# Performance work log

Measured on AMD Instinct MI355X. Metric: run time of the kernel, lower is better.

Reference implementation:

```python
import jax, jax.numpy as jnp
import numpy as np

N = 100000
E = 1600000
IN, HID, OUT = 64, 128, 64
EPS = 1e-5


def _sage_conv(x, src, dst, w_l, b_l, w_r):
    # PyG SAGEConv (mean aggr): out = lin_l(mean_{j in N(i)} x_j) + lin_r(x_i)
    msgs = x[src]                                   # [E, d] gather
    agg = jax.ops.segment_sum(msgs, dst, num_segments=N)  # [N, d]
    deg = jax.ops.segment_sum(jnp.ones((E,), x.dtype), dst, num_segments=N)
    agg = agg / jnp.maximum(deg, 1.0)[:, None]      # mean over neighbors
    return agg @ w_l.T + b_l + x @ w_r.T


def _bn_eval(x, gamma, beta, mean, var):
    return (x - mean) * jax.lax.rsqrt(var + EPS) * gamma + beta


def setup_inputs() -> dict:
    key = jax.random.key(0)
    ks = jax.random.split(key, 16)
    x = jax.random.normal(ks[0], (N, IN), jnp.float32)
    edge_index = jax.random.randint(ks[1], (2, E), 0, N, jnp.int32)
    s1 = 1.0 / np.sqrt(IN)
    s2 = 1.0 / np.sqrt(HID)
    return {
        "x": x,
        "edge_index": edge_index,
        "w1l": jax.random.uniform(ks[2], (HID, IN), jnp.float32, -s1, s1),
        "b1l": jax.random.uniform(ks[3], (HID,), jnp.float32, -s1, s1),
        "w1r": jax.random.uniform(ks[4], (HID, IN), jnp.float32, -s1, s1),
        "bn1_gamma": jax.random.uniform(ks[5], (HID,), jnp.float32, 0.5, 1.5),
        "bn1_beta": jax.random.normal(ks[6], (HID,), jnp.float32) * 0.1,
        "bn1_mean": jax.random.normal(ks[7], (HID,), jnp.float32) * 0.1,
        "bn1_var": jax.random.uniform(ks[8], (HID,), jnp.float32, 0.5, 1.5),
        "w2l": jax.random.uniform(ks[9], (OUT, HID), jnp.float32, -s2, s2),
        "b2l": jax.random.uniform(ks[10], (OUT,), jnp.float32, -s2, s2),
        "w2r": jax.random.uniform(ks[11], (OUT, HID), jnp.float32, -s2, s2),
        "bn2_gamma": jax.random.uniform(ks[12], (OUT,), jnp.float32, 0.5, 1.5),
        "bn2_beta": jax.random.normal(ks[13], (OUT,), jnp.float32) * 0.1,
        "bn2_mean": jax.random.normal(ks[14], (OUT,), jnp.float32) * 0.1,
        "bn2_var": jax.random.uniform(ks[15], (OUT,), jnp.float32, 0.5, 1.5),
    }


def reference(x, edge_index, w1l, b1l, w1r, bn1_gamma, bn1_beta, bn1_mean, bn1_var,
              w2l, b2l, w2r, bn2_gamma, bn2_beta, bn2_mean, bn2_var):
    src, dst = edge_index[0], edge_index[1]
    # layer 1: SAGEConv -> BN -> ReLU (dropout is identity in eval mode)
    h = _sage_conv(x, src, dst, w1l, b1l, w1r)
    h = jax.nn.relu(_bn_eval(h, bn1_gamma, bn1_beta, bn1_mean, bn1_var))
    # layer 2: SAGEConv -> BN
    h = _sage_conv(h, src, dst, w2l, b2l, w2r)
    return _bn_eval(h, bn2_gamma, bn2_beta, bn2_mean, bn2_var)
```

## Files before the change

### kernel.cpp

```cpp
#include <hip/hip_runtime.h>

#define NN 100000
#define NE 1600000
#define EPSV 1e-5f

#define NBUK 196
#define TILE 2048
#define NTIL 782
#define CAP  9216

typedef __attribute__((ext_vector_type(8))) short bf16x8;
typedef __attribute__((ext_vector_type(4))) float f32x4;

__device__ inline unsigned short f2bf(float f) {
  unsigned u = __builtin_bit_cast(unsigned, f);
  unsigned r = u + 0x7FFFu + ((u >> 16) & 1u);
  return (unsigned short)(r >> 16);
}
__device__ inline float bf2f(unsigned short s) {
  unsigned u = ((unsigned)s) << 16;
  return __builtin_bit_cast(float, u);
}

__global__ __launch_bounds__(256) void k_bin(const int* __restrict__ src,
                                             const int* __restrict__ dst,
                                             unsigned* __restrict__ pairs,
                                             int* __restrict__ tileCnt,
                                             int* __restrict__ tileLo) {
  __shared__ int cnt[NBUK];
  __shared__ int lo[NBUK];
  __shared__ int ts[256];
  __shared__ unsigned stage[TILE];
  const int tid = threadIdx.x;
  const int t = blockIdx.x;
  const int e0 = t * TILE;
  const int m = min(TILE, NE - e0);

  for (int i = tid; i < NBUK; i += 256) cnt[i] = 0;
  __syncthreads();
  for (int i = tid; i < m; i += 256) {
    atomicAdd(&cnt[dst[e0 + i] >> 9], 1);
  }
  __syncthreads();
  int c = (tid < NBUK) ? cnt[tid] : 0;
  ts[tid] = c;
  __syncthreads();
  for (int d = 1; d < 256; d <<= 1) {
    int v = (tid >= d) ? ts[tid - d] : 0;
    __syncthreads();
    ts[tid] += v;
    __syncthreads();
  }
  if (tid < NBUK) {
    int ex = ts[tid] - c;
    lo[tid] = ex;
    cnt[tid] = ex;
  }
  __syncthreads();
  for (int i = tid; i < m; i += 256) {
    int d = dst[e0 + i];
    int s = src[e0 + i];
    int pos = atomicAdd(&cnt[d >> 9], 1);
    stage[pos] = ((unsigned)(d & 511) << 17) | (unsigned)s;
  }
  __syncthreads();
  for (int i = tid; i < m; i += 256) pairs[(size_t)t * TILE + i] = stage[i];
  if (tid < NBUK) {
    tileCnt[t * NBUK + tid] = cnt[tid] - lo[tid];
    tileLo[t * NBUK + tid] = lo[tid];
  }
}

__global__ __launch_bounds__(256) void k_colscan(const int* __restrict__ tileCnt,
                                                 int* __restrict__ colBase,
                                                 int* __restrict__ total) {
  __shared__ int ts[256];
  const int tid = threadIdx.x;
  const int b = blockIdx.x;
  int v[4];
  int s = 0;
#pragma unroll
  for (int j = 0; j < 4; ++j) {
    int tt = tid * 4 + j;
    v[j] = (tt < NTIL) ? tileCnt[tt * NBUK + b] : 0;
    s += v[j];
  }
  ts[tid] = s;
  __syncthreads();
  for (int d = 1; d < 256; d <<= 1) {
    int x = (tid >= d) ? ts[tid - d] : 0;
    __syncthreads();
    ts[tid] += x;
    __syncthreads();
  }
  int run = ts[tid] - s;
#pragma unroll
  for (int j = 0; j < 4; ++j) {
    int tt = tid * 4 + j;
    if (tt < NTIL) colBase[(size_t)b * NTIL + tt] = run;
    run += v[j];
  }
  if (tid == 255) total[b] = ts[255];
}

__global__ __launch_bounds__(256) void k_bscan(const int* __restrict__ total,
                                               int* __restrict__ bucketBase) {
  __shared__ int ts[256];
  const int tid = threadIdx.x;
  int c = (tid < NBUK) ? min(total[tid], CAP) : 0;
  ts[tid] = c;
  __syncthreads();
  for (int d = 1; d < 256; d <<= 1) {
    int v = (tid >= d) ? ts[tid - d] : 0;
    __syncthreads();
    ts[tid] += v;
    __syncthreads();
  }
  if (tid < NBUK) bucketBase[tid] = ts[tid] - c;
}

__global__ __launch_bounds__(512) void k_build(const unsigned* __restrict__ pairs,
                                               const int* __restrict__ tileLo,
                                               const int* __restrict__ colBase,
                                               const int* __restrict__ total,
                                               const int* __restrict__ bucketBase,
                                               int* __restrict__ deg,
                                               int* __restrict__ offset,
                                               int* __restrict__ csr) {
  __shared__ unsigned stageA[CAP];
  __shared__ unsigned stageB[CAP];
  __shared__ int colB[NTIL];
  __shared__ int tLo[NTIL];
  __shared__ int hist[512];
  __shared__ int ts[512];
  const int tid = threadIdx.x;
  const int b = blockIdx.x;
  const int count = min(total[b], CAP);
  const int nbase = b * 512;
  const int nloc = min(512, NN - nbase);
  const int obase = bucketBase[b];

  for (int i = tid; i < NTIL; i += 512) {
    colB[i] = colBase[(size_t)b * NTIL + i];
    tLo[i] = tileLo[i * NBUK + b];
  }
  hist[tid] = 0;
  __syncthreads();
  for (int i = tid; i < count; i += 512) {
    int a = 0, z = NTIL - 1;
    while (a < z) {
      int mid = (a + z + 1) >> 1;
      if (colB[mid] <= i) a = mid; else z = mid - 1;
    }
    stageA[i] = pairs[(size_t)a * TILE + tLo[a] + (i - colB[a])];
  }
  __syncthreads();
  for (int i = tid; i < count; i += 512) {
    atomicAdd(&hist[stageA[i] >> 17], 1);
  }
  __syncthreads();
  int s = hist[tid];
  ts[tid] = s;
  __syncthreads();
  for (int d = 1; d < 512; d <<= 1) {
    int v = (tid >= d) ? ts[tid - d] : 0;
    __syncthreads();
    ts[tid] += v;
    __syncthreads();
  }
  int ex = ts[tid] - s;
  if (tid < nloc) {
    deg[nbase + tid] = s;
    offset[nbase + tid] = obase + ex;
  }
  hist[tid] = ex;
  __syncthreads();
  for (int i = tid; i < count; i += 512) {
    unsigned e = stageA[i];
    int pos = atomicAdd(&hist[e >> 17], 1);
    stageB[pos] = e & 0x1FFFFu;
  }
  __syncthreads();
  for (int i = tid; i < count; i += 512) csr[obase + i] = (int)stageB[i];
}

__global__ __launch_bounds__(256) void k_prep(const float* __restrict__ x,
                                              unsigned short* __restrict__ xb,
                                              const float* __restrict__ w1l,
                                              const float* __restrict__ w1r,
                                              const float* __restrict__ w2l,
                                              const float* __restrict__ w2r,
                                              const float* __restrict__ b1l,
                                              const float* __restrict__ g1,
                                              const float* __restrict__ be1,
                                              const float* __restrict__ m1,
                                              const float* __restrict__ v1,
                                              const float* __restrict__ b2l,
                                              const float* __restrict__ g2,
                                              const float* __restrict__ be2,
                                              const float* __restrict__ m2,
                                              const float* __restrict__ v2,
                                              unsigned short* __restrict__ w1c,
                                              unsigned short* __restrict__ w2c,
                                              float* __restrict__ bn) {
  int gi = blockIdx.x * 256 + threadIdx.x;
  float4 v = *(const float4*)(x + (size_t)gi * 4);
  ushort4 o;
  o.x = f2bf(v.x); o.y = f2bf(v.y); o.z = f2bf(v.z); o.w = f2bf(v.w);
  *(ushort4*)(xb + (size_t)gi * 4) = o;
  if (blockIdx.x < 64) {
    int i = gi;
    int oo = i >> 7, k = i & 127;
    float vv1 = (k < 64) ? w1l[oo * 64 + k] : w1r[oo * 64 + (k - 64)];
    w1c[i] = f2bf(vv1);
    float vv2 = (oo < 64) ? w2l[oo * 128 + k] : w2r[(oo - 64) * 128 + k];
    w2c[i] = f2bf(vv2);
    if (i < 128) {
      float sc = g1[i] * rsqrtf(v1[i] + EPSV);
      bn[i] = sc;
      bn[128 + i] = (b1l[i] - m1[i]) * sc + be1[i];
    }
    if (i < 64) {
      float sc = g2[i] * rsqrtf(v2[i] + EPSV);
      bn[256 + i] = sc;
      bn[320 + i] = (b2l[i] - m2[i]) * sc + be2[i];
    }
  }
}

__global__ __launch_bounds__(256) void k_aggregate(const unsigned short* __restrict__ xb,
                                                   const int* __restrict__ deg,
                                                   const int* __restrict__ offset,
                                                   const int* __restrict__ csr,
                                                   unsigned short* __restrict__ aggB) {
  int tid = threadIdx.x;
  int node = blockIdx.x * 32 + (tid >> 3);
  int j = tid & 7;
  int cnt = deg[node];
  const int* arow = csr + offset[node];
  float a0=0.f,a1=0.f,a2=0.f,a3=0.f,a4=0.f,a5=0.f,a6=0.f,a7=0.f;
  int k = 0;
  for (; k + 4 <= cnt; k += 4) {
    int s0 = arow[k], s1 = arow[k+1], s2 = arow[k+2], s3 = arow[k+3];
    uint4 v0 = *(const uint4*)(xb + (size_t)s0 * 64 + j * 8);
    uint4 v1 = *(const uint4*)(xb + (size_t)s1 * 64 + j * 8);
    uint4 v2 = *(const uint4*)(xb + (size_t)s2 * 64 + j * 8);
    uint4 v3 = *(const uint4*)(xb + (size_t)s3 * 64 + j * 8);
    a0 += bf2f(v0.x & 0xffff) + bf2f(v1.x & 0xffff) + bf2f(v2.x & 0xffff) + bf2f(v3.x & 0xffff);
    a1 += bf2f(v0.x >> 16)    + bf2f(v1.x >> 16)    + bf2f(v2.x >> 16)    + bf2f(v3.x >> 16);
    a2 += bf2f(v0.y & 0xffff) + bf2f(v1.y & 0xffff) + bf2f(v2.y & 0xffff) + bf2f(v3.y & 0xffff);
    a3 += bf2f(v0.y >> 16)    + bf2f(v1.y >> 16)    + bf2f(v2.y >> 16)    + bf2f(v3.y >> 16);
    a4 += bf2f(v0.z & 0xffff) + bf2f(v1.z & 0xffff) + bf2f(v2.z & 0xffff) + bf2f(v3.z & 0xffff);
    a5 += bf2f(v0.z >> 16)    + bf2f(v1.z >> 16)    + bf2f(v2.z >> 16)    + bf2f(v3.z >> 16);
    a6 += bf2f(v0.w & 0xffff) + bf2f(v1.w & 0xffff) + bf2f(v2.w & 0xffff) + bf2f(v3.w & 0xffff);
    a7 += bf2f(v0.w >> 16)    + bf2f(v1.w >> 16)    + bf2f(v2.w >> 16)    + bf2f(v3.w >> 16);
  }
  for (; k < cnt; ++k) {
    int s = arow[k];
    uint4 v = *(const uint4*)(xb + (size_t)s * 64 + j * 8);
    a0 += bf2f(v.x & 0xffff); a1 += bf2f(v.x >> 16);
    a2 += bf2f(v.y & 0xffff); a3 += bf2f(v.y >> 16);
    a4 += bf2f(v.z & 0xffff); a5 += bf2f(v.z >> 16);
    a6 += bf2f(v.w & 0xffff); a7 += bf2f(v.w >> 16);
  }
  float inv = 1.0f / fmaxf((float)cnt, 1.0f);
  ushort4 r0, r1;
  r0.x = f2bf(a0 * inv); r0.y = f2bf(a1 * inv); r0.z = f2bf(a2 * inv); r0.w = f2bf(a3 * inv);
  r1.x = f2bf(a4 * inv); r1.y = f2bf(a5 * inv); r1.z = f2bf(a6 * inv); r1.w = f2bf(a7 * inv);
  *(ushort4*)(aggB + (size_t)node * 64 + j * 8) = r0;
  *(ushort4*)(aggB + (size_t)node * 64 + j * 8 + 4) = r1;
}

__global__ __launch_bounds__(256) void k_gemm12(const unsigned short* __restrict__ aggB,
                                                const unsigned short* __restrict__ xb,
                                                const unsigned short* __restrict__ w1c,
                                                const unsigned short* __restrict__ w2c,
                                                const float* __restrict__ bn,
                                                unsigned short* __restrict__ t,
                                                unsigned short* __restrict__ r2) {
  __shared__ unsigned short wlds[32 * 512];
  __shared__ unsigned short hlds[4][2][16 * 128];
  __shared__ float bnlds[384];
  const int tid = threadIdx.x;
  const int w = tid >> 6;
  const int lane = tid & 63;
  const int lr = lane & 15;
  const int q = lane >> 4;
  const int base = blockIdx.x * 128 + w * 32;
  const int nA = base + lr, nB = base + 16 + lr;
  const int cA = min(nA, NN - 1), cB = min(nB, NN - 1);
  const int swz = (lr & 7) << 4;

  bf16x8 fA[4], fB[4];
  {
    const unsigned short* a = aggB + (size_t)cA * 64 + q * 8;
    const unsigned short* xx = xb + (size_t)cA * 64 + q * 8;
    fA[0] = *(const bf16x8*)a;        fA[1] = *(const bf16x8*)(a + 32);
    fA[2] = *(const bf16x8*)xx;       fA[3] = *(const bf16x8*)(xx + 32);
  }
  {
    const unsigned short* a = aggB + (size_t)cB * 64 + q * 8;
    const unsigned short* xx = xb + (size_t)cB * 64 + q * 8;
    fB[0] = *(const bf16x8*)a;        fB[1] = *(const bf16x8*)(a + 32);
    fB[2] = *(const bf16x8*)xx;       fB[3] = *(const bf16x8*)(xx + 32);
  }

  for (int i = tid; i < 384; i += 256) bnlds[i] = bn[i];
  for (int idx = tid; idx < 2048; idx += 256) {
    int f = idx >> 6, l = idx & 63;
    int gofs = ((f >> 2) * 16 + (l & 15)) * 128 + (f & 3) * 32 + (l >> 4) * 8;
    *(uint4*)&wlds[idx * 8] = *(const uint4*)&w1c[gofs];
  }
  __syncthreads();

  char* ldsA = (char*)&hlds[w][0][0];
  char* ldsB = (char*)&hlds[w][1][0];

#pragma unroll
  for (int ot = 0; ot < 8; ++ot) {
    const unsigned short* wp = &wlds[(ot * 4) * 512 + lane * 8];
    bf16x8 w0 = *(const bf16x8*)(wp);
    bf16x8 w1 = *(const bf16x8*)(wp + 512);
    bf16x8 w2 = *(const bf16x8*)(wp + 1024);
    bf16x8 w3 = *(const bf16x8*)(wp + 1536);
    f32x4 aA = {0.f, 0.f, 0.f, 0.f}, aB = {0.f, 0.f, 0.f, 0.f};
    aA = __builtin_amdgcn_mfma_f32_16x16x32_bf16(w0, fA[0], aA, 0, 0, 0);
    aA = __builtin_amdgcn_mfma_f32_16x16x32_bf16(w1, fA[1], aA, 0, 0, 0);
    aA = __builtin_amdgcn_mfma_f32_16x16x32_bf16(w2, fA[2], aA, 0, 0, 0);
    aA = __builtin_amdgcn_mfma_f32_16x16x32_bf16(w3, fA[3], aA, 0, 0, 0);
    aB = __builtin_amdgcn_mfma_f32_16x16x32_bf16(w0, fB[0], aB, 0, 0, 0);
    aB = __builtin_amdgcn_mfma_f32_16x16x32_bf16(w1, fB[1], aB, 0, 0, 0);
    aB = __builtin_amdgcn_mfma_f32_16x16x32_bf16(w2, fB[2], aB, 0, 0, 0);
    aB = __builtin_amdgcn_mfma_f32_16x16x32_bf16(w3, fB[3], aB, 0, 0, 0);
    const int o = ot * 16 + q * 4;
    float4 sc = *(const float4*)&bnlds[o];
    float4 sh = *(const float4*)&bnlds[128 + o];
    ushort4 hA, hB;
    hA.x = f2bf(fmaxf(aA[0] * sc.x + sh.x, 0.f));
    hA.y = f2bf(fmaxf(aA[1] * sc.y + sh.y, 0.f));
    hA.z = f2bf(fmaxf(aA[2] * sc.z + sh.z, 0.f));
    hA.w = f2bf(fmaxf(aA[3] * sc.w + sh.w, 0.f));
    hB.x = f2bf(fmaxf(aB[0] * sc.x + sh.x, 0.f));
    hB.y = f2bf(fmaxf(aB[1] * sc.y + sh.y, 0.f));
    hB.z = f2bf(fmaxf(aB[2] * sc.z + sh.z, 0.f));
    hB.w = f2bf(fmaxf(aB[3] * sc.w + sh.w, 0.f));
    const int wb = lr * 256 + ot * 32 + q * 8;
    *(ushort4*)(ldsA + (wb ^ swz)) = hA;
    *(ushort4*)(ldsB + (wb ^ swz)) = hB;
  }
  __syncthreads();

  for (int idx = tid; idx < 2048; idx += 256) {
    int f = idx >> 6, l = idx & 63;
    int gofs = ((f >> 2) * 16 + (l & 15)) * 128 + (f & 3) * 32 + (l >> 4) * 8;
    *(uint4*)&wlds[idx * 8] = *(const uint4*)&w2c[gofs];
  }
  __syncthreads();

  bf16x8 hA[4], hB[4];
#pragma unroll
  for (int jj = 0; jj < 4; ++jj) {
    const int rb = lr * 256 + jj * 64 + q * 16;
    hA[jj] = *(const bf16x8*)(ldsA + (rb ^ swz));
    hB[jj] = *(const bf16x8*)(ldsB + (rb ^ swz));
  }

#pragma unroll
  for (int ot = 0; ot < 8; ++ot) {
    const unsigned short* wp = &wlds[(ot * 4) * 512 + lane * 8];
    bf16x8 w0 = *(const bf16x8*)(wp);
    bf16x8 w1 = *(const bf16x8*)(wp + 512);
    bf16x8 w2 = *(const bf16x8*)(wp + 1024);
    bf16x8 w3 = *(const bf16x8*)(wp + 1536);
    f32x4 aA = {0.f, 0.f, 0.f, 0.f}, aB = {0.f, 0.f, 0.f, 0.f};
    aA = __builtin_amdgcn_mfma_f32_16x16x32_bf16(w0, hA[0], aA, 0, 0, 0);
    aA = __builtin_amdgcn_mfma_f32_16x16x32_bf16(w1, hA[1], aA, 0, 0, 0);
    aA = __builtin_amdgcn_mfma_f32_16x16x32_bf16(w2, hA[2], aA, 0, 0, 0);
    aA = __builtin_amdgcn_mfma_f32_16x16x32_bf16(w3, hA[3], aA, 0, 0, 0);
    aB = __builtin_amdgcn_mfma_f32_16x16x32_bf16(w0, hB[0], aB, 0, 0, 0);
    aB = __builtin_amdgcn_mfma_f32_16x16x32_bf16(w1, hB[1], aB, 0, 0, 0);
    aB = __builtin_amdgcn_mfma_f32_16x16x32_bf16(w2, hB[2], aB, 0, 0, 0);
    aB = __builtin_amdgcn_mfma_f32_16x16x32_bf16(w3, hB[3], aB, 0, 0, 0);
    ushort4 tv;
    if (ot < 4) {
      const int o = ot * 16 + q * 4;
      tv.x = f2bf(aA[0]); tv.y = f2bf(aA[1]); tv.z = f2bf(aA[2]); tv.w = f2bf(aA[3]);
      if (nA < NN) *(ushort4*)(t + (size_t)nA * 64 + o) = tv;
      tv.x = f2bf(aB[0]); tv.y = f2bf(aB[1]); tv.z = f2bf(aB[2]); tv.w = f2bf(aB[3]);
      if (nB < NN) *(ushort4*)(t + (size_t)nB * 64 + o) = tv;
    } else {
      const int o = (ot - 4) * 16 + q * 4;
      tv.x = f2bf(aA[0]); tv.y = f2bf(aA[1]); tv.z = f2bf(aA[2]); tv.w = f2bf(aA[3]);
      if (nA < NN) *(ushort4*)(r2 + (size_t)nA * 64 + o) = tv;
      tv.x = f2bf(aB[0]); tv.y = f2bf(aB[1]); tv.z = f2bf(aB[2]); tv.w = f2bf(aB[3]);
      if (nB < NN) *(ushort4*)(r2 + (size_t)nB * 64 + o) = tv;
    }
  }
}

__global__ __launch_bounds__(256) void k_agg2fin(const unsigned short* __restrict__ t,
                                                 const int* __restrict__ deg,
                                                 const int* __restrict__ offset,
                                                 const int* __restrict__ csr,
                                                 const unsigned short* __restrict__ r2,
                                                 const float* __restrict__ bn,
                                                 float* __restrict__ outp) {
  int tid = threadIdx.x;
  int node = blockIdx.x * 32 + (tid >> 3);
  int j = tid & 7;
  int cnt = deg[node];
  const int* arow = csr + offset[node];
  float a0=0.f,a1=0.f,a2=0.f,a3=0.f,a4=0.f,a5=0.f,a6=0.f,a7=0.f;
  int k = 0;
  for (; k + 4 <= cnt; k += 4) {
    int s0 = arow[k], s1 = arow[k+1], s2 = arow[k+2], s3 = arow[k+3];
    uint4 v0 = *(const uint4*)(t + (size_t)s0 * 64 + j * 8);
    uint4 v1 = *(const uint4*)(t + (size_t)s1 * 64 + j * 8);
    uint4 v2 = *(const uint4*)(t + (size_t)s2 * 64 + j * 8);
    uint4 v3 = *(const uint4*)(t + (size_t)s3 * 64 + j * 8);
    a0 += bf2f(v0.x & 0xffff) + bf2f(v1.x & 0xffff) + bf2f(v2.x & 0xffff) + bf2f(v3.x & 0xffff);
    a1 += bf2f(v0.x >> 16)    + bf2f(v1.x >> 16)    + bf2f(v2.x >> 16)    + bf2f(v3.x >> 16);
    a2 += bf2f(v0.y & 0xffff) + bf2f(v1.y & 0xffff) + bf2f(v2.y & 0xffff) + bf2f(v3.y & 0xffff);
    a3 += bf2f(v0.y >> 16)    + bf2f(v1.y >> 16)    + bf2f(v2.y >> 16)    + bf2f(v3.y >> 16);
    a4 += bf2f(v0.z & 0xffff) + bf2f(v1.z & 0xffff) + bf2f(v2.z & 0xffff) + bf2f(v3.z & 0xffff);
    a5 += bf2f(v0.z >> 16)    + bf2f(v1.z >> 16)    + bf2f(v2.z >> 16)    + bf2f(v3.z >> 16);
    a6 += bf2f(v0.w & 0xffff) + bf2f(v1.w & 0xffff) + bf2f(v2.w & 0xffff) + bf2f(v3.w & 0xffff);
    a7 += bf2f(v0.w >> 16)    + bf2f(v1.w >> 16)    + bf2f(v2.w >> 16)    + bf2f(v3.w >> 16);
  }
  for (; k < cnt; ++k) {
    int s = arow[k];
    uint4 v = *(const uint4*)(t + (size_t)s * 64 + j * 8);
    a0 += bf2f(v.x & 0xffff); a1 += bf2f(v.x >> 16);
    a2 += bf2f(v.y & 0xffff); a3 += bf2f(v.y >> 16);
    a4 += bf2f(v.z & 0xffff); a5 += bf2f(v.z >> 16);
    a6 += bf2f(v.w & 0xffff); a7 += bf2f(v.w >> 16);
  }
  float inv = 1.0f / fmaxf((float)cnt, 1.0f);
  int o = j * 8;
  uint4 rv = *(const uint4*)(r2 + (size_t)node * 64 + o);
  float r0 = bf2f(rv.x & 0xffff), r1 = bf2f(rv.x >> 16);
  float r2a = bf2f(rv.y & 0xffff), r3 = bf2f(rv.y >> 16);
  float r4 = bf2f(rv.z & 0xffff), r5 = bf2f(rv.z >> 16);
  float r6 = bf2f(rv.w & 0xffff), r7 = bf2f(rv.w >> 16);
  float4 sca = *(const float4*)(bn + 256 + o);
  float4 scb = *(const float4*)(bn + 256 + o + 4);
  float4 sha = *(const float4*)(bn + 320 + o);
  float4 shb = *(const float4*)(bn + 320 + o + 4);
  float4 o0, o1;
  o0.x = (a0 * inv + r0) * sca.x + sha.x;
  o0.y = (a1 * inv + r1) * sca.y + sha.y;
  o0.z = (a2 * inv + r2a) * sca.z + sha.z;
  o0.w = (a3 * inv + r3) * sca.w + sha.w;
  o1.x = (a4 * inv + r4) * scb.x + shb.x;
  o1.y = (a5 * inv + r5) * scb.y + shb.y;
  o1.z = (a6 * inv + r6) * scb.z + shb.z;
  o1.w = (a7 * inv + r7) * scb.w + shb.w;
  *(float4*)(outp + (size_t)node * 64 + o) = o0;
  *(float4*)(outp + (size_t)node * 64 + o + 4) = o1;
}

extern "C" void kernel_launch(void* const* d_in, const int* in_sizes, int n_in,
                              void* d_out, int out_size, void* d_ws, size_t ws_size,
                              hipStream_t stream) {
  const float* x   = (const float*)d_in[0];
  const int*   ei  = (const int*)d_in[1];
  const float* w1l = (const float*)d_in[2];
  const float* b1l = (const float*)d_in[3];
  const float* w1r = (const float*)d_in[4];
  const float* g1  = (const float*)d_in[5];
  const float* be1 = (const float*)d_in[6];
  const float* m1  = (const float*)d_in[7];
  const float* v1  = (const float*)d_in[8];
  const float* w2l = (const float*)d_in[9];
  const float* b2l = (const float*)d_in[10];
  const float* w2r = (const float*)d_in[11];
  const float* g2  = (const float*)d_in[12];
  const float* be2 = (const float*)d_in[13];
  const float* m2  = (const float*)d_in[14];
  const float* v2  = (const float*)d_in[15];
  float* outp = (float*)d_out;

  char* ws = (char*)d_ws;
  int*            tileCnt    = (int*)ws;
  int*            tileLo     = (int*)(ws + 613120);
  int*            colBase    = (int*)(ws + 1226240);
  int*            total      = (int*)(ws + 1839360);
  int*            bucketBase = (int*)(ws + 1840384);
  int*            deg        = (int*)(ws + 1841408);
  int*            offset     = (int*)(ws + 2241408);
  unsigned*       pairs      = (unsigned*)(ws + 2641408);
  int*            csr        = (int*)(ws + 9047552);
  unsigned short* w1c        = (unsigned short*)(ws + 15447552);
  unsigned short* w2c        = (unsigned short*)(ws + 15480320);
  float*          bn         = (float*)(ws + 15513088);
  unsigned short* xb         = (unsigned short*)(ws + 15515136);
  unsigned short* aggB       = (unsigned short*)(ws + 28315136);
  unsigned short* t          = (unsigned short*)(ws + 41115136);
  unsigned short* r2         = (unsigned short*)(ws + 53915136);

  const int* srcp = ei;
  const int* dstp = ei + NE;

  hipLaunchKernelGGL(k_prep, dim3(NN * 64 / 1024), dim3(256), 0, stream,
                     x, xb, w1l, w1r, w2l, w2r, b1l, g1, be1, m1, v1,
                     b2l, g2, be2, m2, v2, w1c, w2c, bn);
  hipLaunchKernelGGL(k_bin, dim3(NTIL), dim3(256), 0, stream,
                     srcp, dstp, pairs, tileCnt, tileLo);
  hipLaunchKernelGGL(k_colscan, dim3(NBUK), dim3(256), 0, stream,
                     tileCnt, colBase, total);
  hipLaunchKernelGGL(k_bscan, dim3(1), dim3(256), 0, stream, total, bucketBase);
  hipLaunchKernelGGL(k_build, dim3(NBUK), dim3(512), 0, stream,
                     pairs, tileLo, colBase, total, bucketBase, deg, offset, csr);
  hipLaunchKernelGGL(k_aggregate, dim3(NN / 32), dim3(256), 0, stream,
                     xb, deg, offset, csr, aggB);
  hipLaunchKernelGGL(k_gemm12, dim3((NN + 127) / 128), dim3(256), 0, stream,
                     aggB, xb, w1c, w2c, bn, t, r2);
  hipLaunchKernelGGL(k_agg2fin, dim3(NN / 32), dim3(256), 0, stream,
                     t, deg, offset, csr, r2, bn, outp);
}
```

Before: 140.4 us.

## Preload both weight matrices into LDS via direct global-to-LDS loads

k_gemm12 now allocates separate LDS buffers for both weight matrices and loads them up front with global_load_lds, removing the mid-kernel reload of w2 and two block barriers. Blocks grow to 512 threads (8 waves) with launch_bounds(512,1), halving the number of blocks that each load the weights. In exchange, LDS use per block roughly doubles, which may cap occupancy. Per-wave h tiles stay private, so the barrier between layers is no longer needed.

```diff
diff --git a/kernel.cpp b/kernel.cpp
--- a/kernel.cpp
+++ b/kernel.cpp
@@ -20,6 +20,12 @@
 __device__ inline float bf2f(unsigned short s) {
   unsigned u = ((unsigned)s) << 16;
   return __builtin_bit_cast(float, u);
+}
+
+__device__ __forceinline__ void gload_lds16(const unsigned short* g, unsigned short* l) {
+  __builtin_amdgcn_global_load_lds(
+      (const __attribute__((address_space(1))) void*)g,
+      (__attribute__((address_space(3))) void*)l, 16, 0, 0);
 }
 
 __global__ __launch_bounds__(256) void k_bin(const int* __restrict__ src,
@@ -271,25 +277,37 @@
   *(ushort4*)(aggB + (size_t)node * 64 + j * 8 + 4) = r1;
 }
 
-__global__ __launch_bounds__(256) void k_gemm12(const unsigned short* __restrict__ aggB,
-                                                const unsigned short* __restrict__ xb,
-                                                const unsigned short* __restrict__ w1c,
-                                                const unsigned short* __restrict__ w2c,
-                                                const float* __restrict__ bn,
-                                                unsigned short* __restrict__ t,
-                                                unsigned short* __restrict__ r2) {
-  __shared__ unsigned short wlds[32 * 512];
-  __shared__ unsigned short hlds[4][2][16 * 128];
+__global__ __launch_bounds__(512, 1) void k_gemm12(const unsigned short* __restrict__ aggB,
+                                                   const unsigned short* __restrict__ xb,
+                                                   const unsigned short* __restrict__ w1c,
+                                                   const unsigned short* __restrict__ w2c,
+                                                   const float* __restrict__ bn,
+                                                   unsigned short* __restrict__ t,
+                                                   unsigned short* __restrict__ r2) {
+  __shared__ unsigned short w1lds[32 * 512];
+  __shared__ unsigned short w2lds[32 * 512];
+  __shared__ unsigned short hlds[8][2][16 * 128];
   __shared__ float bnlds[384];
   const int tid = threadIdx.x;
   const int w = tid >> 6;
   const int lane = tid & 63;
   const int lr = lane & 15;
   const int q = lane >> 4;
-  const int base = blockIdx.x * 128 + w * 32;
+  const int tile = blockIdx.x * 8 + w;
+  const int base = tile * 32;
   const int nA = base + lr, nB = base + 16 + lr;
   const int cA = min(nA, NN - 1), cB = min(nB, NN - 1);
   const int swz = (lr & 7) << 4;
+
+#pragma unroll
+  for (int it = 0; it < 4; ++it) {
+    int idx = it * 512 + tid;
+    int f = idx >> 6, l = idx & 63;
+    int gofs = ((f >> 2) * 16 + (l & 15)) * 128 + (f & 3) * 32 + (l >> 4) * 8;
+    gload_lds16(w1c + gofs, &w1lds[(it * 512 + w * 64) * 8]);
+    gload_lds16(w2c + gofs, &w2lds[(it * 512 + w * 64) * 8]);
+  }
+  if (tid < 384) bnlds[tid] = bn[tid];
 
   bf16x8 fA[4], fB[4];
   {
@@ -304,21 +322,15 @@
     fB[0] = *(const bf16x8*)a;        fB[1] = *(const bf16x8*)(a + 32);
     fB[2] = *(const bf16x8*)xx;       fB[3] = *(const bf16x8*)(xx + 32);
   }
-
-  for (int i = tid; i < 384; i += 256) bnlds[i] = bn[i];
-  for (int idx = tid; idx < 2048; idx += 256) {
-    int f = idx >> 6, l = idx & 63;
-    int gofs = ((f >> 2) * 16 + (l & 15)) * 128 + (f & 3) * 32 + (l >> 4) * 8;
-    *(uint4*)&wlds[idx * 8] = *(const uint4*)&w1c[gofs];
-  }
-  __syncthreads();
+  __syncthreads();
+  if (base >= NN) return;
 
   char* ldsA = (char*)&hlds[w][0][0];
   char* ldsB = (char*)&hlds[w][1][0];
 
 #pragma unroll
   for (int ot = 0; ot < 8; ++ot) {
-    const unsigned short* wp = &wlds[(ot * 4) * 512 + lane * 8];
+    const unsigned short* wp = &w1lds[(ot * 4) * 512 + lane * 8];
     bf16x8 w0 = *(const bf16x8*)(wp);
     bf16x8 w1 = *(const bf16x8*)(wp + 512);
     bf16x8 w2 = *(const bf16x8*)(wp + 1024);
@@ -348,14 +360,6 @@
     *(ushort4*)(ldsA + (wb ^ swz)) = hA;
     *(ushort4*)(ldsB + (wb ^ swz)) = hB;
   }
-  __syncthreads();
-
-  for (int idx = tid; idx < 2048; idx += 256) {
-    int f = idx >> 6, l = idx & 63;
-    int gofs = ((f >> 2) * 16 + (l & 15)) * 128 + (f & 3) * 32 + (l >> 4) * 8;
-    *(uint4*)&wlds[idx * 8] = *(const uint4*)&w2c[gofs];
-  }
-  __syncthreads();
 
   bf16x8 hA[4], hB[4];
 #pragma unroll
@@ -367,7 +371,7 @@
 
 #pragma unroll
   for (int ot = 0; ot < 8; ++ot) {
-    const unsigned short* wp = &wlds[(ot * 4) * 512 + lane * 8];
+    const unsigned short* wp = &w2lds[(ot * 4) * 512 + lane * 8];
     bf16x8 w0 = *(const bf16x8*)(wp);
     bf16x8 w1 = *(const bf16x8*)(wp + 512);
     bf16x8 w2 = *(const bf16x8*)(wp + 1024);
@@ -513,7 +517,7 @@
                      pairs, tileLo, colBase, total, bucketBase, deg, offset, csr);
   hipLaunchKernelGGL(k_aggregate, dim3(NN / 32), dim3(256), 0, stream,
                      xb, deg, offset, csr, aggB);
-  hipLaunchKernelGGL(k_gemm12, dim3((NN + 127) / 128), dim3(256), 0, stream,
+  hipLaunchKernelGGL(k_gemm12, dim3((NN / 32 + 7) / 8), dim3(512), 0, stream,
                      aggB, xb, w1c, w2c, bn, t, r2);
   hipLaunchKernelGGL(k_agg2fin, dim3(NN / 32), dim3(256), 0, stream,
                      t, deg, offset, csr, r2, bn, outp);
```

Result: faster. 135.4 us (-3.5%).
